# Kernel tuning notes

Measured on AMD Instinct MI355X. Metric: run time of the kernel, lower is better.

The kernel has to match this reference:

```python
import jax, jax.numpy as jnp
import numpy as np

N_NODES = 100000
N_EDGES = 3200000
D_IN = 128
D_OUT = 128


def setup_inputs() -> dict:
    key = jax.random.key(0)
    kx, kw, kb, kr, kc, kv = jax.random.split(key, 6)
    x = jax.random.normal(kx, (N_NODES, D_IN), dtype=jnp.float32)
    W = jax.random.normal(kw, (D_OUT, D_IN), dtype=jnp.float32) * (1.0 / np.sqrt(D_IN))
    b = jax.random.normal(kb, (D_OUT,), dtype=jnp.float32) * 0.01
    adj_rows = jax.random.randint(kr, (N_EDGES,), 0, N_NODES, dtype=jnp.int32)
    adj_cols = jax.random.randint(kc, (N_EDGES,), 0, N_NODES, dtype=jnp.int32)
    adj_vals = jax.random.uniform(kv, (N_EDGES,), dtype=jnp.float32)
    return {"x": x, "W": W, "b": b, "adj_rows": adj_rows,
            "adj_cols": adj_cols, "adj_vals": adj_vals}


def reference(x, W, b, adj_rows, adj_cols, adj_vals):
    # linear: out = x @ W.T + b   -> [N, D_OUT]
    out = jnp.einsum('ni,oi->no', x, W) + b
    # spmm(adj, out): row r = sum over edges (r, c, v) of v * out[c]
    gathered = out[adj_cols] * adj_vals[:, None]          # [E, D_OUT]
    agg = jax.ops.segment_sum(gathered, adj_rows, num_segments=x.shape[0])
    return jax.nn.elu(agg)
```

## Files before the change

kernel.cpp:

```cpp
#include <hip/hip_runtime.h>
#include <hip/hip_bf16.h>
#include <cmath>

#define RPB      32
#define FB_CAP   1280
#define SB_SHIFT 11
#define NSB_MAX  64
#define TILE     2048
#define CH_PER_SB 34
#define CPAD     32

typedef __attribute__((ext_vector_type(8))) short short8;
typedef __attribute__((ext_vector_type(4))) float floatx4;

__device__ __forceinline__ unsigned short f2bf(float f) {
    unsigned int u = __float_as_uint(f);
    u += 0x7FFFu + ((u >> 16) & 1u);
    return (unsigned short)(u >> 16);
}

__device__ __forceinline__ void gemm_body(
    char* smraw, const float* __restrict__ x,
    const unsigned short* __restrict__ Wbg, const float* __restrict__ b,
    unsigned short* __restrict__ Yb, int N, int blk)
{
    unsigned short* Wb = (unsigned short*)smraw;
    unsigned short* Xb = Wb + 128 * 136;
    const int t    = threadIdx.x;
    const int wave = t >> 6;
    const int lane = t & 63;
    const int col  = lane & 15;
    const int quad = lane >> 4;
    const int rowbase = blk * 64;

#pragma unroll
    for (int i = 0; i < 8; ++i) {
        const int idx = t + 256 * i;
        const int o = idx >> 4, k8 = (idx & 15) * 8;
        *(uint4*)&Wb[o * 136 + k8] = *(const uint4*)&Wbg[idx * 8];
    }
#pragma unroll
    for (int i = 0; i < 8; ++i) {
        const int idx = t + 256 * i;
        const int row = idx >> 5, k4 = (idx & 31) * 4;
        const int gr = rowbase + row;
        float4 v = make_float4(0.f, 0.f, 0.f, 0.f);
        if (gr < N) v = *(const float4*)&x[(size_t)gr * 128 + k4];
        Xb[row * 136 + k4 + 0] = f2bf(v.x); Xb[row * 136 + k4 + 1] = f2bf(v.y);
        Xb[row * 136 + k4 + 2] = f2bf(v.z); Xb[row * 136 + k4 + 3] = f2bf(v.w);
    }
    __syncthreads();

    float bias[8];
#pragma unroll
    for (int nt = 0; nt < 8; ++nt) bias[nt] = b[nt * 16 + col];

    floatx4 acc[8] = {};
    const int mrow = wave * 16;
#pragma unroll
    for (int k0 = 0; k0 < 128; k0 += 32) {
        const short8 a = *(const short8*)&Xb[(mrow + col) * 136 + k0 + quad * 8];
#pragma unroll
        for (int nt = 0; nt < 8; ++nt) {
            const short8 bf = *(const short8*)&Wb[(nt * 16 + col) * 136 + k0 + quad * 8];
            acc[nt] = __builtin_amdgcn_mfma_f32_16x16x32_bf16(a, bf, acc[nt], 0, 0, 0);
        }
    }
#pragma unroll
    for (int nt = 0; nt < 8; ++nt) {
#pragma unroll
        for (int reg = 0; reg < 4; ++reg)
            Xb[(mrow + quad * 4 + reg) * 136 + nt * 16 + col] =
                f2bf(acc[nt][reg] + bias[nt]);
    }
    __syncthreads();
#pragma unroll
    for (int i = 0; i < 4; ++i) {
        const int idx = t + 256 * i;
        const int row = idx >> 4, c16 = (idx & 15) * 8;
        const int gr  = rowbase + row;
        if (gr < N)
            *(uint4*)&Yb[(size_t)gr * 128 + c16] = *(const uint4*)&Xb[row * 136 + c16];
    }
}

__device__ __forceinline__ void pass1_body(
    char* smraw, const int* __restrict__ rows, const int* __restrict__ cols,
    const float* __restrict__ vals, int* __restrict__ cursor1,
    int2* __restrict__ pairs1, int E, int blk)
{
    int2* sbuf           = (int2*)smraw;
    unsigned char* sbin  = (unsigned char*)(sbuf + TILE);
    unsigned short* perm = (unsigned short*)(sbin + TILE);
    int* hist  = (int*)(perm + TILE);
    int* off   = hist + NSB_MAX;
    int* gbase = off + NSB_MAX;
    int* cur   = gbase + NSB_MAX;
    const int t  = threadIdx.x;
    const int lane = t & 63;
    const int lo = blk * TILE;
    const int cnt = min(TILE, E - lo);

    if (t < NSB_MAX) hist[t] = 0;
    __syncthreads();
    for (int i = t; i < cnt; i += 256) {
        const int   r = rows[lo + i];
        const int   c = cols[lo + i];
        const float v = vals[lo + i];
        sbuf[i] = make_int2(((r & 2047) << 17) | c, __float_as_int(v));
        const int bb = r >> SB_SHIFT;
        sbin[i] = (unsigned char)bb;
        atomicAdd(&hist[bb], 1);
    }
    __syncthreads();
    if (t < NSB_MAX) {
        const int h = hist[t];
        int s = h;
#pragma unroll
        for (int d = 1; d < NSB_MAX; d <<= 1) {
            const int n = __shfl_up(s, d);
            if (lane >= d) s += n;
        }
        off[t] = s - h;
        cur[t] = s - h;
        if (h > 0) gbase[t] = atomicAdd(&cursor1[t * CPAD], h);
    }
    __syncthreads();
    for (int i = t; i < cnt; i += 256) {
        const int pos = atomicAdd(&cur[sbin[i]], 1);
        perm[pos] = (unsigned short)i;
    }
    __syncthreads();
    for (int i = t; i < cnt; i += 256) {
        const int src = perm[i];
        const int bb  = sbin[src];
        pairs1[gbase[bb] + (i - off[bb])] = sbuf[src];
    }
}

__global__ __launch_bounds__(256) void fused_gemm_pass1_kernel(
    const float* __restrict__ x, const unsigned short* __restrict__ Wbg,
    const float* __restrict__ b, unsigned short* __restrict__ Yb, int N, int GB,
    const int* __restrict__ rows, const int* __restrict__ cols,
    const float* __restrict__ vals, int* __restrict__ cursor1,
    int2* __restrict__ pairs1, int E, int PB)
{
    extern __shared__ __align__(16) char smraw[];
    const int bid = blockIdx.x;
    const int mn  = min(GB, PB);
    int type, sub;
    if (bid < 2 * mn) { type = bid & 1; sub = bid >> 1; }
    else              { type = (GB > PB) ? 0 : 1; sub = mn + (bid - 2 * mn); }
    if (type == 0) gemm_body(smraw, x, Wbg, b, Yb, N, sub);
    else           pass1_body(smraw, rows, cols, vals, cursor1, pairs1, E, sub);
}

__global__ __launch_bounds__(256) void gemm_mfma_kernel(
    const float* __restrict__ x, const unsigned short* __restrict__ Wbg,
    const float* __restrict__ b, unsigned short* __restrict__ Yb, int N)
{
    __shared__ __align__(16) char sm[(128 * 136 + 64 * 136) * 2];
    gemm_body(sm, x, Wbg, b, Yb, N, blockIdx.x);
}

__global__ __launch_bounds__(256) void pass1_kernel(
    const int* __restrict__ rows, const int* __restrict__ cols,
    const float* __restrict__ vals, int* __restrict__ cursor1,
    int2* __restrict__ pairs1, int E)
{
    __shared__ __align__(16) char sm[TILE * 8 + TILE + TILE * 2 + NSB_MAX * 16];
    pass1_body(sm, rows, cols, vals, cursor1, pairs1, E, blockIdx.x);
}

__global__ __launch_bounds__(256) void init_cursor_kernel(
    int* __restrict__ cursor1, int* __restrict__ cursor2, int SB_CAP, int NB,
    const float* __restrict__ W, unsigned short* __restrict__ Wbg)
{
    const int i = blockIdx.x * blockDim.x + threadIdx.x;
    if (i < NSB_MAX) cursor1[i * CPAD] = i * SB_CAP;
    if (i < NB)      cursor2[i] = i * FB_CAP;
    const int stride = gridDim.x * blockDim.x;
    for (int j = i; j < 128 * 128 / 4; j += stride) {
        const float4 v = ((const float4*)W)[j];
        uint2 u;
        u.x = (unsigned)f2bf(v.x) | ((unsigned)f2bf(v.y) << 16);
        u.y = (unsigned)f2bf(v.z) | ((unsigned)f2bf(v.w) << 16);
        ((uint2*)Wbg)[j] = u;
    }
}

__global__ __launch_bounds__(256) void pass2_kernel(
    const int* __restrict__ cursor1, int* __restrict__ cursor2,
    const int2* __restrict__ pairs1, int2* __restrict__ pairs2, int SB_CAP)
{
    __shared__ int2 sbuf[TILE];
    __shared__ unsigned short perm[TILE];
    __shared__ int hist[64], off[64], gbase[64], cur[64];
    const int t   = threadIdx.x;
    const int lane = t & 63;
    const int sb  = blockIdx.x / CH_PER_SB;
    const int ch  = blockIdx.x % CH_PER_SB;
    const int base = sb * SB_CAP;
    const int scnt = cursor1[sb * CPAD] - base;
    const int csz  = (scnt + CH_PER_SB - 1) / CH_PER_SB;
    const int lo   = ch * csz;
    const int cnt  = max(0, min(csz, scnt - lo));

    if (t < 64) hist[t] = 0;
    __syncthreads();
    for (int i = t; i < cnt; i += 256) {
        const int2 p = pairs1[base + lo + i];
        sbuf[i] = p;
        atomicAdd(&hist[(unsigned)p.x >> 22], 1);
    }
    __syncthreads();
    if (t < 64) {
        const int h = hist[t];
        int s = h;
#pragma unroll
        for (int d = 1; d < 64; d <<= 1) {
            const int n = __shfl_up(s, d);
            if (lane >= d) s += n;
        }
        off[t] = s - h;
        cur[t] = s - h;
        if (h > 0) gbase[t] = atomicAdd(&cursor2[sb * 64 + t], h);
    }
    __syncthreads();
    for (int i = t; i < cnt; i += 256) {
        const int pos = atomicAdd(&cur[(unsigned)sbuf[i].x >> 22], 1);
        perm[pos] = (unsigned short)i;
    }
    __syncthreads();
    for (int i = t; i < cnt; i += 256) {
        const int2 p = sbuf[perm[i]];
        const int bb = (unsigned)p.x >> 22;
        pairs2[gbase[bb] + (i - off[bb])] = make_int2(p.x & 0x3FFFFF, p.y);
    }
}

__global__ __launch_bounds__(256) void sortgather_kernel(
    const int* __restrict__ cursor2, const int2* __restrict__ pairs2,
    const unsigned int* __restrict__ Yu, float* __restrict__ out, int N)
{
    __shared__ __align__(16) int2 sbuf[FB_CAP];
    __shared__ __align__(16) int2 dbuf[FB_CAP + 4];
    __shared__ int hist[RPB];
    __shared__ int off[RPB];
    __shared__ int cur[RPB];
    __shared__ int rowtick;
    const int b    = blockIdx.x;
    const int t    = threadIdx.x;
    const int lane = t & 63;
    const int slot = b * FB_CAP;
    int cnt = cursor2[b] - slot;
    if (cnt > FB_CAP) cnt = FB_CAP;

    if (t < RPB) hist[t] = 0;
    if (t == 0) rowtick = 0;
    __syncthreads();
    for (int i = t; i < cnt; i += 256) {
        const int2 p = pairs2[slot + i];
        sbuf[i] = p;
        atomicAdd(&hist[p.x >> 17], 1);
    }
    __syncthreads();
    if (t == 0) {
        int run = 0;
#pragma unroll
        for (int k = 0; k < RPB; ++k) { off[k] = run; cur[k] = run; run += hist[k]; }
    }
    __syncthreads();
    for (int i = t; i < cnt; i += 256) {
        const int2 p   = sbuf[i];
        const int  pos = atomicAdd(&cur[p.x >> 17], 1);
        dbuf[pos] = make_int2(p.x & 0x1FFFF, p.y);
    }
    if (t < 4) dbuf[cnt + t] = make_int2(0, 0);
    __syncthreads();

    const int sub   = lane >> 4;
    const int qlane = lane & 15;

    for (;;) {
        int rl = 0;
        if (lane == 0) rl = atomicAdd(&rowtick, 1);
        rl = __shfl(rl, 0);
        if (rl >= RPB) break;
        const int gr = b * RPB + rl;
        if (gr >= N) continue;
        const int s = off[rl];
        const int e = s + hist[rl];

        float acc0 = 0.f, acc1 = 0.f, acc2 = 0.f, acc3 = 0.f;
        float acc4 = 0.f, acc5 = 0.f, acc6 = 0.f, acc7 = 0.f;
#pragma unroll 2
        for (int j = s; j < e; j += 4) {
            const int2 p = dbuf[j + sub];
            float v = __int_as_float(p.y);
            v = (j + sub < e) ? v : 0.0f;
            const uint4 y = *(const uint4*)&Yu[((unsigned)p.x << 6) + qlane * 4];
            acc0 = fmaf(v, __uint_as_float(y.x << 16), acc0);
            acc1 = fmaf(v, __uint_as_float(y.x & 0xFFFF0000u), acc1);
            acc2 = fmaf(v, __uint_as_float(y.y << 16), acc2);
            acc3 = fmaf(v, __uint_as_float(y.y & 0xFFFF0000u), acc3);
            acc4 = fmaf(v, __uint_as_float(y.z << 16), acc4);
            acc5 = fmaf(v, __uint_as_float(y.z & 0xFFFF0000u), acc5);
            acc6 = fmaf(v, __uint_as_float(y.w << 16), acc6);
            acc7 = fmaf(v, __uint_as_float(y.w & 0xFFFF0000u), acc7);
        }
        acc0 += __shfl_xor(acc0, 32); acc1 += __shfl_xor(acc1, 32);
        acc2 += __shfl_xor(acc2, 32); acc3 += __shfl_xor(acc3, 32);
        acc4 += __shfl_xor(acc4, 32); acc5 += __shfl_xor(acc5, 32);
        acc6 += __shfl_xor(acc6, 32); acc7 += __shfl_xor(acc7, 32);
        acc0 += __shfl_xor(acc0, 16); acc1 += __shfl_xor(acc1, 16);
        acc2 += __shfl_xor(acc2, 16); acc3 += __shfl_xor(acc3, 16);
        acc4 += __shfl_xor(acc4, 16); acc5 += __shfl_xor(acc5, 16);
        acc6 += __shfl_xor(acc6, 16); acc7 += __shfl_xor(acc7, 16);

        if (lane < 16) {
            float4 o0, o1;
            o0.x = acc0 > 0.f ? acc0 : __expf(acc0) - 1.f;
            o0.y = acc1 > 0.f ? acc1 : __expf(acc1) - 1.f;
            o0.z = acc2 > 0.f ? acc2 : __expf(acc2) - 1.f;
            o0.w = acc3 > 0.f ? acc3 : __expf(acc3) - 1.f;
            o1.x = acc4 > 0.f ? acc4 : __expf(acc4) - 1.f;
            o1.y = acc5 > 0.f ? acc5 : __expf(acc5) - 1.f;
            o1.z = acc6 > 0.f ? acc6 : __expf(acc6) - 1.f;
            o1.w = acc7 > 0.f ? acc7 : __expf(acc7) - 1.f;
            float* po = &out[(size_t)gr * 128 + qlane * 8];
            *(float4*)po       = o0;
            *(float4*)(po + 4) = o1;
        }
    }
}

__global__ __launch_bounds__(256) void gemm_bias_kernel(
    const float* __restrict__ x, const float* __restrict__ W,
    const float* __restrict__ b, float* __restrict__ Y, int N)
{
    __shared__ float Wt[128][130];
    const int tid  = threadIdx.x;
    const int wave = tid >> 6;
    const int lane = tid & 63;
    for (int i = tid; i < 128 * 128; i += 256) {
        const int o = i >> 7, k = i & 127;
        Wt[k][o] = W[i];
    }
    __syncthreads();
    const float2 bv = *(const float2*)&b[2 * lane];
    for (int row = blockIdx.x * 4 + wave; row < N; row += gridDim.x * 4) {
        float acc0 = 0.f, acc1 = 0.f;
        for (int k = 0; k < 128; ++k) {
            const float2 w = *(const float2*)&Wt[k][2 * lane];
            const float xv = x[(size_t)row * 128 + k];
            acc0 = fmaf(xv, w.x, acc0);
            acc1 = fmaf(xv, w.y, acc1);
        }
        float2 o2; o2.x = acc0 + bv.x; o2.y = acc1 + bv.y;
        *(float2*)&Y[(size_t)row * 128 + 2 * lane] = o2;
    }
}

__global__ __launch_bounds__(256) void scatter_kernel(
    const int* __restrict__ rows, const int* __restrict__ cols,
    const float* __restrict__ vals, const float* __restrict__ Y,
    float* __restrict__ out, int E)
{
    const long long gid = (long long)blockIdx.x * blockDim.x + threadIdx.x;
    const int wid  = (int)(gid >> 6);
    const int lane = threadIdx.x & 63;
    if (wid >= E) return;
    const int   r = rows[wid];
    const int   c = cols[wid];
    const float v = vals[wid];
    const float2 y = *(const float2*)&Y[(size_t)c * 128 + 2 * lane];
    float* po = &out[(size_t)r * 128 + 2 * lane];
    atomicAdd(po,     v * y.x);
    atomicAdd(po + 1, v * y.y);
}

__global__ __launch_bounds__(256) void elu_kernel(float* __restrict__ out, int n4)
{
    int i = blockIdx.x * blockDim.x + threadIdx.x;
    const int stride = gridDim.x * blockDim.x;
    float4* p = (float4*)out;
    for (; i < n4; i += stride) {
        float4 v = p[i];
        v.x = v.x > 0.f ? v.x : expf(v.x) - 1.f;
        v.y = v.y > 0.f ? v.y : expf(v.y) - 1.f;
        v.z = v.z > 0.f ? v.z : expf(v.z) - 1.f;
        v.w = v.w > 0.f ? v.w : expf(v.w) - 1.f;
        p[i] = v;
    }
}

extern "C" void kernel_launch(void* const* d_in, const int* in_sizes, int n_in,
                              void* d_out, int out_size, void* d_ws, size_t ws_size,
                              hipStream_t stream)
{
    const float* x    = (const float*)d_in[0];
    const float* W    = (const float*)d_in[1];
    const float* b    = (const float*)d_in[2];
    const int*   rows = (const int*)d_in[3];
    const int*   cols = (const int*)d_in[4];
    const float* vals = (const float*)d_in[5];
    float* out = (float*)d_out;

    const int N   = in_sizes[0] / 128;
    const int E   = in_sizes[3];
    const int NB  = (N + RPB - 1) / RPB;
    const int NSB = (N + (1 << SB_SHIFT) - 1) >> SB_SHIFT;

    const int sb_mean = (E + NSB - 1) / NSB;
    int sbsig = 1; while (sbsig * sbsig < sb_mean) ++sbsig;
    const int SB_CAP = (sb_mean + 10 * sbsig + 63) & ~63;

    auto align256 = [](size_t v) { return (v + 255) & ~(size_t)255; };
    const size_t offPairs2 = 0;
    const size_t szPairs2  = (size_t)NB * FB_CAP * 8;
    const size_t offShared = align256(offPairs2 + szPairs2);
    const size_t szPairs1  = (size_t)NSB * SB_CAP * 8;
    const size_t szY       = (size_t)N * 256;
    const size_t szShared  = szPairs1 > szY ? szPairs1 : szY;
    const size_t offCur1_a = align256(offShared + szShared);
    const size_t offCur2_a = align256(offCur1_a + (size_t)NSB_MAX * 4 * CPAD);
    const size_t offWb_a   = align256(offCur2_a + (size_t)NB * 4);
    const size_t need      = offWb_a + 128 * 128 * 2;
    const size_t offPairs1 = offShared;
    const size_t offY      = align256(offPairs1 + szPairs1);
    const size_t offCur1_o = align256(offY + szY);
    const size_t offCur2_o = align256(offCur1_o + (size_t)NSB_MAX * 4 * CPAD);
    const size_t offWb_o   = align256(offCur2_o + (size_t)NB * 4);
    const size_t need_ovl  = offWb_o + 128 * 128 * 2;

    const bool csr_ok = (need <= ws_size) && (NSB <= NSB_MAX) &&
                        ((long long)E <= (long long)NB * 1056) &&
                        (SB_CAP <= CH_PER_SB * TILE);
    const bool ovl_ok = csr_ok && (need_ovl <= ws_size);

    if (ovl_ok) {
        int2* pairs2        = (int2*)((char*)d_ws + offPairs2);
        int2* pairs1        = (int2*)((char*)d_ws + offPairs1);
        unsigned short* Yb  = (unsigned short*)((char*)d_ws + offY);
        int*  cursor1       = (int*)((char*)d_ws + offCur1_o);
        int*  cursor2       = (int*)((char*)d_ws + offCur2_o);
        unsigned short* Wbg = (unsigned short*)((char*)d_ws + offWb_o);

        const int GB = (N + 63) / 64;
        const int PB = (E + TILE - 1) / TILE;
        const int smsz = (128 * 136 + 64 * 136) * 2;

        init_cursor_kernel<<<(NB + 255) / 256, 256, 0, stream>>>(cursor1, cursor2,
                                                                 SB_CAP, NB, W, Wbg);
        fused_gemm_pass1_kernel<<<GB + PB, 256, smsz, stream>>>(
            x, Wbg, b, Yb, N, GB, rows, cols, vals, cursor1, pairs1, E, PB);
        pass2_kernel<<<NSB * CH_PER_SB, 256, 0, stream>>>(cursor1, cursor2,
                                                          pairs1, pairs2, SB_CAP);
        sortgather_kernel<<<NB, 256, 0, stream>>>(cursor2, pairs2,
                                                  (const unsigned int*)Yb, out, N);
    } else if (csr_ok) {
        int2* pairs2        = (int2*)((char*)d_ws + offPairs2);
        int2* pairs1        = (int2*)((char*)d_ws + offShared);
        unsigned short* Yb  = (unsigned short*)((char*)d_ws + offShared);
        int*  cursor1       = (int*)((char*)d_ws + offCur1_a);
        int*  cursor2       = (int*)((char*)d_ws + offCur2_a);
        unsigned short* Wbg = (unsigned short*)((char*)d_ws + offWb_a);

        init_cursor_kernel<<<(NB + 255) / 256, 256, 0, stream>>>(cursor1, cursor2,
                                                                 SB_CAP, NB, W, Wbg);
        pass1_kernel<<<(E + TILE - 1) / TILE, 256, 0, stream>>>(rows, cols, vals,
                                                                cursor1, pairs1, E);
        pass2_kernel<<<NSB * CH_PER_SB, 256, 0, stream>>>(cursor1, cursor2,
                                                          pairs1, pairs2, SB_CAP);
        gemm_mfma_kernel<<<(N + 63) / 64, 256, 0, stream>>>(x, Wbg, b, Yb, N);
        sortgather_kernel<<<NB, 256, 0, stream>>>(cursor2, pairs2,
                                                  (const unsigned int*)Yb, out, N);
    } else {
        float* Y = (float*)d_ws;
        hipMemsetAsync(d_out, 0, (size_t)out_size * sizeof(float), stream);
        gemm_bias_kernel<<<512, 256, 0, stream>>>(x, W, b, Y, N);
        scatter_kernel<<<(E + 3) / 4, 256, 0, stream>>>(rows, cols, vals, Y, out, E);
        elu_kernel<<<1024, 256, 0, stream>>>(out, out_size / 4);
    }
}
```

Before: 283.2 us.

## Load GEMM operands directly to registers and drop sortgather staging buffer

The GEMM body now reads x straight from global memory into MFMA A-fragments in registers and reads bf16 W from global/L2 instead of staging both in LDS, keeping LDS only for the output epilogue. This shrinks the fused kernel's dynamic shared memory to the pass1 requirement, which raises occupancy for both block types. Sortgather also drops its sbuf staging array and re-reads pairs2 from global a second time, halving its LDS use. The cost is uncoalesced per-lane x loads, repeated W reads from cache by every block, and a duplicate global read of pairs2.

Result: slower. 302.4 us (+6.8%).

```diff
diff --git a/kernel.cpp b/kernel.cpp
--- a/kernel.cpp
+++ b/kernel.cpp
@@ -24,53 +24,57 @@
     const unsigned short* __restrict__ Wbg, const float* __restrict__ b,
     unsigned short* __restrict__ Yb, int N, int blk)
 {
-    unsigned short* Wb = (unsigned short*)smraw;
-    unsigned short* Xb = Wb + 128 * 136;
+    unsigned short* Eb = (unsigned short*)smraw;
     const int t    = threadIdx.x;
     const int wave = t >> 6;
     const int lane = t & 63;
     const int col  = lane & 15;
     const int quad = lane >> 4;
     const int rowbase = blk * 64;
-
-#pragma unroll
-    for (int i = 0; i < 8; ++i) {
-        const int idx = t + 256 * i;
-        const int o = idx >> 4, k8 = (idx & 15) * 8;
-        *(uint4*)&Wb[o * 136 + k8] = *(const uint4*)&Wbg[idx * 8];
-    }
-#pragma unroll
-    for (int i = 0; i < 8; ++i) {
-        const int idx = t + 256 * i;
-        const int row = idx >> 5, k4 = (idx & 31) * 4;
-        const int gr = rowbase + row;
-        float4 v = make_float4(0.f, 0.f, 0.f, 0.f);
-        if (gr < N) v = *(const float4*)&x[(size_t)gr * 128 + k4];
-        Xb[row * 136 + k4 + 0] = f2bf(v.x); Xb[row * 136 + k4 + 1] = f2bf(v.y);
-        Xb[row * 136 + k4 + 2] = f2bf(v.z); Xb[row * 136 + k4 + 3] = f2bf(v.w);
-    }
-    __syncthreads();
+    const int mrow = wave * 16;
+
+    short8 af[4];
+    const int arow = rowbase + mrow + col;
+    if (arow < N) {
+#pragma unroll
+        for (int kk = 0; kk < 4; ++kk) {
+            const float4 v0 = *(const float4*)&x[(size_t)arow * 128 + kk * 32 + quad * 8];
+            const float4 v1 = *(const float4*)&x[(size_t)arow * 128 + kk * 32 + quad * 8 + 4];
+            short8 a;
+            a[0] = (short)f2bf(v0.x); a[1] = (short)f2bf(v0.y);
+            a[2] = (short)f2bf(v0.z); a[3] = (short)f2bf(v0.w);
+            a[4] = (short)f2bf(v1.x); a[5] = (short)f2bf(v1.y);
+            a[6] = (short)f2bf(v1.z); a[7] = (short)f2bf(v1.w);
+            af[kk] = a;
+        }
+    } else {
+#pragma unroll
+        for (int kk = 0; kk < 4; ++kk) {
+            short8 a;
+#pragma unroll
+            for (int j = 0; j < 8; ++j) a[j] = 0;
+            af[kk] = a;
+        }
+    }
 
     float bias[8];
 #pragma unroll
     for (int nt = 0; nt < 8; ++nt) bias[nt] = b[nt * 16 + col];
 
     floatx4 acc[8] = {};
-    const int mrow = wave * 16;
-#pragma unroll
-    for (int k0 = 0; k0 < 128; k0 += 32) {
-        const short8 a = *(const short8*)&Xb[(mrow + col) * 136 + k0 + quad * 8];
+#pragma unroll
+    for (int kk = 0; kk < 4; ++kk) {
 #pragma unroll
         for (int nt = 0; nt < 8; ++nt) {
-            const short8 bf = *(const short8*)&Wb[(nt * 16 + col) * 136 + k0 + quad * 8];
-            acc[nt] = __builtin_amdgcn_mfma_f32_16x16x32_bf16(a, bf, acc[nt], 0, 0, 0);
+            const short8 bf = *(const short8*)&Wbg[(nt * 16 + col) * 128 + kk * 32 + quad * 8];
+            acc[nt] = __builtin_amdgcn_mfma_f32_16x16x32_bf16(af[kk], bf, acc[nt], 0, 0, 0);
         }
     }
 #pragma unroll
     for (int nt = 0; nt < 8; ++nt) {
 #pragma unroll
         for (int reg = 0; reg < 4; ++reg)
-            Xb[(mrow + quad * 4 + reg) * 136 + nt * 16 + col] =
+            Eb[(mrow + quad * 4 + reg) * 136 + nt * 16 + col] =
                 f2bf(acc[nt][reg] + bias[nt]);
     }
     __syncthreads();
@@ -80,7 +84,7 @@
         const int row = idx >> 4, c16 = (idx & 15) * 8;
         const int gr  = rowbase + row;
         if (gr < N)
-            *(uint4*)&Yb[(size_t)gr * 128 + c16] = *(const uint4*)&Xb[row * 136 + c16];
+            *(uint4*)&Yb[(size_t)gr * 128 + c16] = *(const uint4*)&Eb[row * 136 + c16];
     }
 }
 
@@ -159,7 +163,7 @@
     const float* __restrict__ x, const unsigned short* __restrict__ Wbg,
     const float* __restrict__ b, unsigned short* __restrict__ Yb, int N)
 {
-    __shared__ __align__(16) char sm[(128 * 136 + 64 * 136) * 2];
+    __shared__ __align__(16) char sm[64 * 136 * 2];
     gemm_body(sm, x, Wbg, b, Yb, N, blockIdx.x);
 }
 
@@ -243,7 +247,6 @@
     const int* __restrict__ cursor2, const int2* __restrict__ pairs2,
     const unsigned int* __restrict__ Yu, float* __restrict__ out, int N)
 {
-    __shared__ __align__(16) int2 sbuf[FB_CAP];
     __shared__ __align__(16) int2 dbuf[FB_CAP + 4];
     __shared__ int hist[RPB];
     __shared__ int off[RPB];
@@ -260,9 +263,7 @@
     if (t == 0) rowtick = 0;
     __syncthreads();
     for (int i = t; i < cnt; i += 256) {
-        const int2 p = pairs2[slot + i];
-        sbuf[i] = p;
-        atomicAdd(&hist[p.x >> 17], 1);
+        atomicAdd(&hist[pairs2[slot + i].x >> 17], 1);
     }
     __syncthreads();
     if (t == 0) {
@@ -272,7 +273,7 @@
     }
     __syncthreads();
     for (int i = t; i < cnt; i += 256) {
-        const int2 p   = sbuf[i];
+        const int2 p   = pairs2[slot + i];
         const int  pos = atomicAdd(&cur[p.x >> 17], 1);
         dbuf[pos] = make_int2(p.x & 0x1FFFF, p.y);
     }
@@ -449,7 +450,7 @@
 
         const int GB = (N + 63) / 64;
         const int PB = (E + TILE - 1) / TILE;
-        const int smsz = (128 * 136 + 64 * 136) * 2;
+        const int smsz = TILE * 8 + TILE + TILE * 2 + NSB_MAX * 16;
 
         init_cursor_kernel<<<(NB + 255) / 256, 256, 0, stream>>>(cursor1, cursor2,
                                                                  SB_CAP, NB, W, Wbg);
```
